# Kernel tuning notes

Measured on AMD Instinct MI355X. Metric: run time of the kernel, lower is better.

Reference implementation:

```python
import jax, jax.numpy as jnp
import numpy as np

N_NODES = 50000
N_EDGES = 600000
D = 128
NUM_GRAPHS = 64


def gcn_conv(x, W, b, edge_index, edge_weight, n):
    """PyG GCNConv: y = D^-1/2 (A+I) D^-1/2 (x W) + b, with self-loop weight 1."""
    h = x @ W  # [n, out]
    src, dst = edge_index[0], edge_index[1]
    if edge_weight is None:
        edge_weight = jnp.ones(src.shape, dtype=x.dtype)
    # append self loops
    loop = jnp.arange(n)
    src_f = jnp.concatenate([src, loop])
    dst_f = jnp.concatenate([dst, loop])
    w_f = jnp.concatenate([edge_weight, jnp.ones((n,), dtype=x.dtype)])
    deg = jax.ops.segment_sum(w_f, dst_f, num_segments=n)
    dis = jnp.where(deg > 0, jax.lax.rsqrt(jnp.maximum(deg, 1e-12)), 0.0)
    norm = dis[src_f] * w_f * dis[dst_f]  # [E+n]
    msg = h[src_f] * norm[:, None]
    out = jax.ops.segment_sum(msg, dst_f, num_segments=n)
    return out + b


def setup_inputs() -> dict:
    key = jax.random.key(0)
    ks = jax.random.split(key, 24)
    def w(k, shape, scale=0.05):
        return jax.random.normal(k, shape, dtype=jnp.float32) * scale
    inp = {
        'x': jax.random.normal(ks[0], (N_NODES, D), dtype=jnp.float32),
        'edge_index': jax.random.randint(ks[1], (2, N_EDGES), 0, N_NODES),
        'edge_attr': jax.random.uniform(ks[2], (N_EDGES, 4), dtype=jnp.float32),
        'batch': jnp.sort(jax.random.randint(ks[3], (N_NODES,), 0, NUM_GRAPHS)),
        'W1A': w(ks[4], (D, D)), 'b1A': jnp.zeros((D,), jnp.float32),
        'W1B': w(ks[5], (D, D)), 'b1B': jnp.zeros((D,), jnp.float32),
        'W1C': w(ks[6], (D, D)), 'b1C': jnp.zeros((D,), jnp.float32),
        'W1D': w(ks[7], (D, D)), 'b1D': jnp.zeros((D,), jnp.float32),
        'W2': w(ks[8], (4 * D, 2 * D)), 'b2': jnp.zeros((2 * D,), jnp.float32),
        'W3': w(ks[9], (2 * D, D)), 'b3': jnp.zeros((D,), jnp.float32),
        'Wm1': w(ks[10], (2 * D, 8)), 'bm1': jnp.zeros((8,), jnp.float32),
        'Wm2': w(ks[11], (8, 2)), 'bm2': jnp.zeros((2,), jnp.float32),
    }
    return inp


def reference(x, edge_index, edge_attr, batch, W1A, b1A, W1B, b1B, W1C, b1C,
              W1D, b1D, W2, b2, W3, b3, Wm1, bm1, Wm2, bm2):
    n = x.shape[0]
    xA = jax.nn.relu(gcn_conv(x, W1A, b1A, edge_index, edge_attr[:, 0], n))
    xB = jax.nn.relu(gcn_conv(x, W1B, b1B, edge_index, edge_attr[:, 1], n))
    xC = jax.nn.relu(gcn_conv(x, W1C, b1C, edge_index, edge_attr[:, 2], n))
    xD = jax.nn.relu(gcn_conv(x, W1D, b1D, edge_index, edge_attr[:, 3], n))
    h = jnp.concatenate([xA, xB, xC, xD], axis=1)  # [n, 4D]
    h = jax.nn.relu(gcn_conv(h, W2, b2, edge_index, None, n))
    h = gcn_conv(h, W3, b3, edge_index, None, n)  # [n, D]
    # global mean / max pool over graphs
    counts = jax.ops.segment_sum(jnp.ones((n,), h.dtype), batch, num_segments=NUM_GRAPHS)
    sums = jax.ops.segment_sum(h, batch, num_segments=NUM_GRAPHS)
    mean = sums / jnp.maximum(counts, 1.0)[:, None]
    mx = jax.ops.segment_max(h, batch, num_segments=NUM_GRAPHS)
    mx = jnp.where(counts[:, None] > 0, mx, 0.0)
    g = jnp.concatenate([mean, mx], axis=1)  # [G, 2D]
    # dropout is identity in eval mode
    logits = jax.nn.relu(g @ Wm1 + bm1) @ Wm2 + bm2
    return logits
```

## Files before the change

kernel.cpp:

```cpp
#include <hip/hip_runtime.h>

#define DEV_INLINE __device__ __forceinline__

typedef __attribute__((ext_vector_type(8))) short bf16x8;
typedef __attribute__((ext_vector_type(4))) float floatx4;

DEV_INLINE unsigned fencode(float f) {
  unsigned u = __float_as_uint(f);
  return (u & 0x80000000u) ? ~u : (u | 0x80000000u);
}
DEV_INLINE float fdecode(unsigned k) {
  return __uint_as_float((k & 0x80000000u) ? (k ^ 0x80000000u) : ~k);
}

DEV_INLINE unsigned short bf16_rne(float x) {
  unsigned u = __float_as_uint(x);
  unsigned r = (u + 0x7FFFu + ((u >> 16) & 1u)) >> 16;
  return (unsigned short)r;
}
DEV_INLINE void bf16_split(float x, unsigned short& hi, unsigned short& lo) {
  hi = bf16_rne(x);
  float hf = __uint_as_float(((unsigned)hi) << 16);
  lo = bf16_rne(x - hf);
}
DEV_INLINE float bf2f(unsigned short u) {
  return __uint_as_float(((unsigned)u) << 16);
}

#pragma clang diagnostic ignored "-Waddress-space-conversion"
DEV_INLINE void gload_lds16(const void* g, void* l) {
  __builtin_amdgcn_global_load_lds(
      (const __attribute__((address_space(1))) unsigned int*)g,
      (__attribute__((address_space(3))) unsigned int*)l, 16, 0, 0);
}

__global__ __launch_bounds__(256)
void prep_kernel(const float* __restrict__ WA, const float* __restrict__ WB,
                 const float* __restrict__ WC, const float* __restrict__ WD,
                 const float* __restrict__ bA, const float* __restrict__ bB,
                 const float* __restrict__ bC, const float* __restrict__ bD,
                 const float* __restrict__ W2, const float* __restrict__ W3,
                 unsigned short* __restrict__ W1t_hi, unsigned short* __restrict__ W1t_lo,
                 unsigned short* __restrict__ W2t_hi, unsigned short* __restrict__ W2t_lo,
                 unsigned short* __restrict__ W3t_hi, unsigned short* __restrict__ W3t_lo,
                 float* __restrict__ biascat) {
  int i = blockIdx.x * 256 + threadIdx.x;
  if (i < 65536) {
    int z = i >> 14, rem = i & 16383, j = rem >> 7, k = rem & 127;
    const float* W = (z == 0) ? WA : (z == 1) ? WB : (z == 2) ? WC : WD;
    unsigned short hi, lo;
    bf16_split(W[k * 128 + j], hi, lo);
    W1t_hi[i] = hi; W1t_lo[i] = lo;
  } else if (i < 196608) {
    int i2 = i - 65536, j = i2 >> 9, k = i2 & 511;
    unsigned short hi, lo;
    bf16_split(W2[k * 256 + j], hi, lo);
    W2t_hi[i2] = hi; W2t_lo[i2] = lo;
  } else if (i < 229376) {
    int i3 = i - 196608, j = i3 >> 8, k = i3 & 255;
    unsigned short hi, lo;
    bf16_split(W3[k * 128 + j], hi, lo);
    W3t_hi[i3] = hi; W3t_lo[i3] = lo;
  } else if (i < 229888) {
    int i4 = i - 229376, c = i4 >> 7, j = i4 & 127;
    const float* b = (c == 0) ? bA : (c == 1) ? bB : (c == 2) ? bC : bD;
    biascat[i4] = b[j];
  }
}

__global__ __launch_bounds__(256)
void xcast_kernel(const float* __restrict__ x, unsigned short* __restrict__ xb, int total4) {
  int i = blockIdx.x * 256 + threadIdx.x;
  if (i >= total4) return;
  float4 v = ((const float4*)x)[i];
  ushort4 o;
  o.x = bf16_rne(v.x); o.y = bf16_rne(v.y); o.z = bf16_rne(v.z); o.w = bf16_rne(v.w);
  ((ushort4*)xb)[i] = o;
}

__global__ __launch_bounds__(256)
void hist_kernel(const int* __restrict__ ei, int* __restrict__ cnt, int E) {
  int e = blockIdx.x * 256 + threadIdx.x;
  if (e < E) atomicAdd(&cnt[ei[E + e]], 1);
}

__global__ __launch_bounds__(256)
void scan1_kernel(const int* __restrict__ cnt, int* __restrict__ local,
                  int* __restrict__ bsum, int n) {
  __shared__ int s[256];
  int tid = threadIdx.x;
  int i = blockIdx.x * 256 + tid;
  int v = (i < n) ? cnt[i] : 0;
  s[tid] = v;
  __syncthreads();
#pragma unroll
  for (int off = 1; off < 256; off <<= 1) {
    int t = (tid >= off) ? s[tid - off] : 0;
    __syncthreads();
    s[tid] += t;
    __syncthreads();
  }
  if (i < n) local[i] = s[tid] - v;
  if (tid == 255) bsum[blockIdx.x] = s[255];
}

__global__ __launch_bounds__(256)
void scan2_kernel(int* __restrict__ bsum, int nb) {
  __shared__ int s[256];
  int tid = threadIdx.x;
  int v = (tid < nb) ? bsum[tid] : 0;
  s[tid] = v;
  __syncthreads();
#pragma unroll
  for (int off = 1; off < 256; off <<= 1) {
    int t = (tid >= off) ? s[tid - off] : 0;
    __syncthreads();
    s[tid] += t;
    __syncthreads();
  }
  if (tid < nb) bsum[tid] = s[tid] - v;
}

__global__ __launch_bounds__(256)
void scan3_kernel(const int* __restrict__ local, const int* __restrict__ bsum,
                  int* __restrict__ rowptr, int* __restrict__ rowwork, int n, int E) {
  int i = blockIdx.x * 256 + threadIdx.x;
  if (i < n) {
    int rp = local[i] + bsum[blockIdx.x];
    rowptr[i] = rp;
    rowwork[i] = rp;
  }
  if (i == 0) rowptr[n] = E;
}

__global__ __launch_bounds__(256)
void fill_kernel(const int* __restrict__ ei, int* __restrict__ rowwork,
                 int* __restrict__ csr, int* __restrict__ csr_src,
                 int* __restrict__ csr_dst, int E) {
  int e = blockIdx.x * 256 + threadIdx.x;
  if (e >= E) return;
  int d = ei[E + e];
  int pos = atomicAdd(&rowwork[d], 1);
  csr[pos] = e;
  csr_src[pos] = ei[e];
  csr_dst[pos] = d;
}

__global__ __launch_bounds__(256)
void degcsr_kernel(const int* __restrict__ rowptr, const int* __restrict__ csr,
                   const float* __restrict__ eattr, float* __restrict__ dis, int n) {
  int d = blockIdx.x * 256 + threadIdx.x;
  if (d >= n) return;
  int beg = rowptr[d], end = rowptr[d + 1];
  float s0 = 1.f, s1 = 1.f, s2 = 1.f, s3 = 1.f;
  for (int i = beg; i < end; ++i) {
    int e = csr[i];
    float4 w = ((const float4*)eattr)[e];
    s0 += w.x; s1 += w.y; s2 += w.z; s3 += w.w;
  }
  dis[d]         = 1.0f / sqrtf(s0);
  dis[n + d]     = 1.0f / sqrtf(s1);
  dis[2 * n + d] = 1.0f / sqrtf(s2);
  dis[3 * n + d] = 1.0f / sqrtf(s3);
  dis[4 * n + d] = 1.0f / sqrtf(1.0f + (float)(end - beg));
}

__global__ __launch_bounds__(256)
void edgeprep_kernel(const int* __restrict__ csr, const int* __restrict__ csr_src,
                     const int* __restrict__ csr_dst, const float* __restrict__ eattr,
                     const float* __restrict__ dis, float4* __restrict__ norm4,
                     float* __restrict__ norm1, int n, int E) {
  int i = blockIdx.x * 256 + threadIdx.x;
  if (i >= E) return;
  int e = csr[i], s = csr_src[i], d = csr_dst[i];
  float4 w = ((const float4*)eattr)[e];
  float4 o;
  o.x = dis[s] * w.x * dis[d];
  o.y = dis[n + s] * w.y * dis[n + d];
  o.z = dis[2 * n + s] * w.z * dis[2 * n + d];
  o.w = dis[3 * n + s] * w.w * dis[3 * n + d];
  norm4[i] = o;
  norm1[i] = dis[4 * n + s] * dis[4 * n + d];
}

__global__ __launch_bounds__(256)
void agg4x_kernel(const unsigned short* __restrict__ xb,
                  unsigned short* __restrict__ xa,
                  const int* __restrict__ rowptr, const int* __restrict__ csr_src,
                  const float4* __restrict__ norm4, const float* __restrict__ dis,
                  int n, int npad) {
  int d = blockIdx.x * 4 + (threadIdx.x >> 6);
  if (d >= n) return;
  int t = threadIdx.x & 63;
  float dc0 = dis[d], dc1 = dis[n + d], dc2 = dis[2 * n + d], dc3 = dis[3 * n + d];
  const ushort2* x2 = (const ushort2*)xb;
  ushort2 xu = x2[(size_t)d * 64 + t];
  float xvx = bf2f(xu.x), xvy = bf2f(xu.y);
  float a0x = xvx * dc0 * dc0, a0y = xvy * dc0 * dc0;
  float a1x = xvx * dc1 * dc1, a1y = xvy * dc1 * dc1;
  float a2x = xvx * dc2 * dc2, a2y = xvy * dc2 * dc2;
  float a3x = xvx * dc3 * dc3, a3y = xvy * dc3 * dc3;
  int beg = rowptr[d], end = rowptr[d + 1];
  int i = beg;
  for (; i + 4 <= end; i += 4) {
    int s0 = csr_src[i], s1 = csr_src[i + 1], s2 = csr_src[i + 2], s3 = csr_src[i + 3];
    float4 m0 = norm4[i], m1 = norm4[i + 1], m2 = norm4[i + 2], m3 = norm4[i + 3];
    ushort2 u0 = x2[(size_t)s0 * 64 + t];
    ushort2 u1 = x2[(size_t)s1 * 64 + t];
    ushort2 u2 = x2[(size_t)s2 * 64 + t];
    ushort2 u3 = x2[(size_t)s3 * 64 + t];
    float h0x = bf2f(u0.x), h0y = bf2f(u0.y);
    float h1x = bf2f(u1.x), h1y = bf2f(u1.y);
    float h2x = bf2f(u2.x), h2y = bf2f(u2.y);
    float h3x = bf2f(u3.x), h3y = bf2f(u3.y);
    a0x += h0x * m0.x; a0y += h0y * m0.x;
    a1x += h0x * m0.y; a1y += h0y * m0.y;
    a2x += h0x * m0.z; a2y += h0y * m0.z;
    a3x += h0x * m0.w; a3y += h0y * m0.w;
    a0x += h1x * m1.x; a0y += h1y * m1.x;
    a1x += h1x * m1.y; a1y += h1y * m1.y;
    a2x += h1x * m1.z; a2y += h1y * m1.z;
    a3x += h1x * m1.w; a3y += h1y * m1.w;
    a0x += h2x * m2.x; a0y += h2y * m2.x;
    a1x += h2x * m2.y; a1y += h2y * m2.y;
    a2x += h2x * m2.z; a2y += h2y * m2.z;
    a3x += h2x * m2.w; a3y += h2y * m2.w;
    a0x += h3x * m3.x; a0y += h3y * m3.x;
    a1x += h3x * m3.y; a1y += h3y * m3.y;
    a2x += h3x * m3.z; a2y += h3y * m3.z;
    a3x += h3x * m3.w; a3y += h3y * m3.w;
  }
  for (; i < end; ++i) {
    int s = csr_src[i];
    float4 m = norm4[i];
    ushort2 u = x2[(size_t)s * 64 + t];
    float hx = bf2f(u.x), hy = bf2f(u.y);
    a0x += hx * m.x; a0y += hy * m.x;
    a1x += hx * m.y; a1y += hy * m.y;
    a2x += hx * m.z; a2y += hy * m.z;
    a3x += hx * m.w; a3y += hy * m.w;
  }
  size_t plane = (size_t)npad * 128;
  size_t base = (size_t)d * 128 + 2 * t;
  float vx[4] = {a0x, a1x, a2x, a3x};
  float vy[4] = {a0y, a1y, a2y, a3y};
#pragma unroll
  for (int z = 0; z < 4; ++z) {
    ushort2 ov; ov.x = bf16_rne(vx[z]); ov.y = bf16_rne(vy[z]);
    *(ushort2*)&xa[plane * z + base] = ov;
  }
}

template <int MODE>
DEV_INLINE void gemm_mfma_body(const unsigned short* __restrict__ Ab, int K,
                               const unsigned short* __restrict__ Bh,
                               const unsigned short* __restrict__ Bl, int nTile0,
                               int ldc, int col0, unsigned short* __restrict__ Cb,
                               const float* __restrict__ bias, int M, int row0) {
  __shared__ __align__(16) unsigned short As[128 * 32];
  __shared__ __align__(16) unsigned short Bsh[128 * 32];
  __shared__ __align__(16) unsigned short Bsl[128 * 32];
  int tid = threadIdx.x;
  int w = tid >> 6, lane = tid & 63;
  int quad = lane >> 4, lrow = lane & 15;
  int wm = (w >> 1) * 64, wn = (w & 1) * 64;

  floatx4 zero4 = {0.f, 0.f, 0.f, 0.f};
  floatx4 acc[4][4];
#pragma unroll
  for (int i = 0; i < 4; ++i)
#pragma unroll
    for (int j = 0; j < 4; ++j) acc[i][j] = zero4;

  for (int k0 = 0; k0 < K; k0 += 32) {
#pragma unroll
    for (int half = 0; half < 2; ++half) {
      int row = half * 64 + lane;
      size_t ga = (size_t)(row0 + row) * K + k0 + w * 8;
      size_t gb = (size_t)(nTile0 + row) * K + k0 + w * 8;
      int lb = (w * 128 + half * 64) * 8;
      gload_lds16(Ab + ga, &As[lb]);
      gload_lds16(Bh + gb, &Bsh[lb]);
      gload_lds16(Bl + gb, &Bsl[lb]);
    }
    __syncthreads();
    bf16x8 ah[4];
#pragma unroll
    for (int i = 0; i < 4; ++i) {
      int off = (quad * 128 + wm + i * 16 + lrow) * 8;
      ah[i] = *(const bf16x8*)&As[off];
    }
#pragma unroll
    for (int j = 0; j < 4; ++j) {
      int off = (quad * 128 + wn + j * 16 + lrow) * 8;
      bf16x8 bh = *(const bf16x8*)&Bsh[off];
      bf16x8 bl = *(const bf16x8*)&Bsl[off];
#pragma unroll
      for (int i = 0; i < 4; ++i) {
        acc[i][j] = __builtin_amdgcn_mfma_f32_16x16x32_bf16(ah[i], bh, acc[i][j], 0, 0, 0);
        acc[i][j] = __builtin_amdgcn_mfma_f32_16x16x32_bf16(ah[i], bl, acc[i][j], 0, 0, 0);
      }
    }
    __syncthreads();
  }
#pragma unroll
  for (int i = 0; i < 4; ++i) {
#pragma unroll
    for (int j = 0; j < 4; ++j) {
      int colL = wn + j * 16 + lrow;
#pragma unroll
      for (int r = 0; r < 4; ++r) {
        int row = row0 + wm + i * 16 + quad * 4 + r;
        if (row < M) {
          float v = acc[i][j][r];
          if (MODE == 1) v = fmaxf(v + bias[colL], 0.0f);
          Cb[(size_t)row * ldc + col0 + colL] = bf16_rne(v);
        }
      }
    }
  }
}

__global__ __launch_bounds__(256)
void gemm_l1_mfma(const unsigned short* __restrict__ xa,
                  const unsigned short* __restrict__ W1t_hi,
                  const unsigned short* __restrict__ W1t_lo,
                  const float* __restrict__ biascat,
                  unsigned short* __restrict__ h1, int M, int npad) {
  int z = blockIdx.z;
  size_t ap = (size_t)z * npad * 128;
  gemm_mfma_body<1>(xa + ap, 128, W1t_hi + z * 16384, W1t_lo + z * 16384, 0,
                    512, z * 128, h1, biascat + z * 128, M, blockIdx.x * 128);
}

__global__ __launch_bounds__(256)
void gemm_bf16out(const unsigned short* __restrict__ Ab, int K,
                  const unsigned short* __restrict__ Bh,
                  const unsigned short* __restrict__ Bl,
                  unsigned short* __restrict__ Cb, int ldc, int M) {
  gemm_mfma_body<2>(Ab, K, Bh, Bl, blockIdx.y * 128, ldc, blockIdx.y * 128,
                    Cb, nullptr, M, blockIdx.x * 128);
}

template <int VEC, bool RELU, int OMODE>
__global__ __launch_bounds__(256)
void agg1_kernel(const unsigned short* __restrict__ hb, float* __restrict__ out,
                 unsigned short* __restrict__ ob,
                 const int* __restrict__ rowptr, const int* __restrict__ csr_src,
                 const float* __restrict__ norm1, const float* __restrict__ dis1,
                 const float* __restrict__ bias, int n) {
  constexpr int DOUT = VEC * 64;
  int d = blockIdx.x * 4 + (threadIdx.x >> 6);
  if (d >= n) return;
  int t = threadIdx.x & 63;
  float dd = dis1[d];
  float acc[VEC];
  {
    float sw = dd * dd;
#pragma unroll
    for (int k = 0; k < VEC; ++k) acc[k] = bf2f(hb[(size_t)d * DOUT + t * VEC + k]) * sw;
  }
  int beg = rowptr[d], end = rowptr[d + 1];
  int i = beg;
  for (; i + 4 <= end; i += 4) {
    int s0 = csr_src[i], s1 = csr_src[i + 1], s2 = csr_src[i + 2], s3 = csr_src[i + 3];
    float m0 = norm1[i], m1 = norm1[i + 1], m2 = norm1[i + 2], m3 = norm1[i + 3];
    if (VEC == 4) {
      ushort4 u0 = *(const ushort4*)&hb[(size_t)s0 * DOUT + t * 4];
      ushort4 u1 = *(const ushort4*)&hb[(size_t)s1 * DOUT + t * 4];
      ushort4 u2 = *(const ushort4*)&hb[(size_t)s2 * DOUT + t * 4];
      ushort4 u3 = *(const ushort4*)&hb[(size_t)s3 * DOUT + t * 4];
      acc[0] += bf2f(u0.x) * m0; acc[1] += bf2f(u0.y) * m0;
      acc[2 % VEC] += bf2f(u0.z) * m0; acc[3 % VEC] += bf2f(u0.w) * m0;
      acc[0] += bf2f(u1.x) * m1; acc[1] += bf2f(u1.y) * m1;
      acc[2 % VEC] += bf2f(u1.z) * m1; acc[3 % VEC] += bf2f(u1.w) * m1;
      acc[0] += bf2f(u2.x) * m2; acc[1] += bf2f(u2.y) * m2;
      acc[2 % VEC] += bf2f(u2.z) * m2; acc[3 % VEC] += bf2f(u2.w) * m2;
      acc[0] += bf2f(u3.x) * m3; acc[1] += bf2f(u3.y) * m3;
      acc[2 % VEC] += bf2f(u3.z) * m3; acc[3 % VEC] += bf2f(u3.w) * m3;
    } else {
      ushort2 u0 = *(const ushort2*)&hb[(size_t)s0 * DOUT + t * 2];
      ushort2 u1 = *(const ushort2*)&hb[(size_t)s1 * DOUT + t * 2];
      ushort2 u2 = *(const ushort2*)&hb[(size_t)s2 * DOUT + t * 2];
      ushort2 u3 = *(const ushort2*)&hb[(size_t)s3 * DOUT + t * 2];
      acc[0] += bf2f(u0.x) * m0; acc[1 % VEC] += bf2f(u0.y) * m0;
      acc[0] += bf2f(u1.x) * m1; acc[1 % VEC] += bf2f(u1.y) * m1;
      acc[0] += bf2f(u2.x) * m2; acc[1 % VEC] += bf2f(u2.y) * m2;
      acc[0] += bf2f(u3.x) * m3; acc[1 % VEC] += bf2f(u3.y) * m3;
    }
  }
  for (; i < end; ++i) {
    int s = csr_src[i];
    float nrm = norm1[i];
    if (VEC == 4) {
      ushort4 u = *(const ushort4*)&hb[(size_t)s * DOUT + t * 4];
      acc[0] += bf2f(u.x) * nrm; acc[1] += bf2f(u.y) * nrm;
      acc[2 % VEC] += bf2f(u.z) * nrm; acc[3 % VEC] += bf2f(u.w) * nrm;
    } else {
      ushort2 u = *(const ushort2*)&hb[(size_t)s * DOUT + t * 2];
      acc[0] += bf2f(u.x) * nrm; acc[1 % VEC] += bf2f(u.y) * nrm;
    }
  }
#pragma unroll
  for (int k = 0; k < VEC; ++k) {
    float r = acc[k] + bias[t * VEC + k];
    if (RELU) r = fmaxf(r, 0.0f);
    if (OMODE == 1) {
      ob[(size_t)d * DOUT + t * VEC + k] = bf16_rne(r);
    } else {
      out[(size_t)d * DOUT + t * VEC + k] = r;
    }
  }
}

__global__ __launch_bounds__(128)
void pool_kernel(const float* __restrict__ h3, const int* __restrict__ batch,
                 float* __restrict__ gsum, unsigned* __restrict__ gmax, int n) {
  int c = threadIdx.x;
  int start = blockIdx.x * 32;
  int end = min(start + 32, n);
  int curg = -1;
  float s = 0.0f, m = -3.402823466e38f;
  for (int i = start; i < end; ++i) {
    int g = batch[i];
    if (g != curg) {
      if (curg >= 0) {
        atomicAdd(&gsum[curg * 128 + c], s);
        atomicMax(&gmax[curg * 128 + c], fencode(m));
      }
      curg = g; s = 0.0f; m = -3.402823466e38f;
    }
    float v = h3[(size_t)i * 128 + c];
    s += v;
    m = fmaxf(m, v);
  }
  if (curg >= 0) {
    atomicAdd(&gsum[curg * 128 + c], s);
    atomicMax(&gmax[curg * 128 + c], fencode(m));
  }
}

__global__ __launch_bounds__(512)
void mlp_kernel(const float* __restrict__ gsum, const unsigned* __restrict__ gmax,
                const int* __restrict__ batch, int n, const float* __restrict__ Wm1,
                const float* __restrict__ bm1, const float* __restrict__ Wm2,
                const float* __restrict__ bm2, float* __restrict__ out) {
  __shared__ float hid[64][8];
  int t = threadIdx.x;
  int gi = t >> 3, u = t & 7;
  auto lb = [&](int key) {
    int lo = 0, hi = n;
    while (lo < hi) {
      int mid = (lo + hi) >> 1;
      if (batch[mid] < key) lo = mid + 1; else hi = mid;
    }
    return lo;
  };
  int cnt = lb(gi + 1) - lb(gi);
  float inv = 1.0f / fmaxf((float)cnt, 1.0f);
  float s = bm1[u];
  for (int k = 0; k < 128; ++k) {
    float mean = gsum[gi * 128 + k] * inv;
    s += mean * Wm1[k * 8 + u];
  }
  for (int k = 0; k < 128; ++k) {
    float mx = (cnt > 0) ? fdecode(gmax[gi * 128 + k]) : 0.0f;
    s += mx * Wm1[(128 + k) * 8 + u];
  }
  hid[gi][u] = fmaxf(s, 0.0f);
  __syncthreads();
  if (t < 128) {
    int g2 = t >> 1, o = t & 1;
    float s2 = bm2[o];
#pragma unroll
    for (int uu = 0; uu < 8; ++uu) s2 += hid[g2][uu] * Wm2[uu * 2 + o];
    out[g2 * 2 + o] = s2;
  }
}

extern "C" void kernel_launch(void* const* d_in, const int* in_sizes, int n_in,
                              void* d_out, int out_size, void* d_ws, size_t ws_size,
                              hipStream_t stream) {
  const float* x     = (const float*)d_in[0];
  const int*   ei    = (const int*)d_in[1];
  const float* eattr = (const float*)d_in[2];
  const int*   batch = (const int*)d_in[3];
  const float* W1A = (const float*)d_in[4],  *b1A = (const float*)d_in[5];
  const float* W1B = (const float*)d_in[6],  *b1B = (const float*)d_in[7];
  const float* W1C = (const float*)d_in[8],  *b1C = (const float*)d_in[9];
  const float* W1D = (const float*)d_in[10], *b1D = (const float*)d_in[11];
  const float* W2  = (const float*)d_in[12], *b2  = (const float*)d_in[13];
  const float* W3  = (const float*)d_in[14], *b3  = (const float*)d_in[15];
  const float* Wm1 = (const float*)d_in[16], *bm1 = (const float*)d_in[17];
  const float* Wm2 = (const float*)d_in[18], *bm2 = (const float*)d_in[19];
  float* out = (float*)d_out;

  const int n = in_sizes[0] / 128;
  const int E = in_sizes[1] / 2;
  const int npad = (n + 127) & ~127;
  const int nmb = npad / 128;

  char* ws = (char*)d_ws;
  size_t off = 0;
  auto alloc = [&](size_t bytes) -> void* {
    void* p = ws + off;
    off += (bytes + 255) & ~(size_t)255;
    return p;
  };

  float*    dis     = (float*)alloc((size_t)5 * n * 4);
  int*      rowptr  = (int*)alloc(((size_t)n + 1) * 4);
  int*      rowwork = (int*)alloc((size_t)n * 4);
  int*      local   = (int*)alloc((size_t)n * 4);
  int*      bsum    = (int*)alloc(256 * 4);
  size_t zoff = off;
  int*      cnt     = (int*)alloc((size_t)n * 4);
  float*    gsum    = (float*)alloc(64 * 128 * 4);
  unsigned* gmax    = (unsigned*)alloc(64 * 128 * 4);
  size_t zbytes = off - zoff;
  int*      csr     = (int*)alloc((size_t)E * 4);
  int*      csr_src = (int*)alloc((size_t)E * 4);
  int*      csr_dst = (int*)alloc((size_t)E * 4);
  float4*   norm4   = (float4*)alloc((size_t)E * 16);
  float*    norm1   = (float*)alloc((size_t)E * 4);
  unsigned short* W1t_hi = (unsigned short*)alloc(65536 * 2);
  unsigned short* W1t_lo = (unsigned short*)alloc(65536 * 2);
  unsigned short* W2t_hi = (unsigned short*)alloc(131072 * 2);
  unsigned short* W2t_lo = (unsigned short*)alloc(131072 * 2);
  unsigned short* W3t_hi = (unsigned short*)alloc(32768 * 2);
  unsigned short* W3t_lo = (unsigned short*)alloc(32768 * 2);
  float*    biascat = (float*)alloc(512 * 4);
  unsigned short* xb   = (unsigned short*)alloc((size_t)npad * 128 * 2);
  unsigned short* bufA = (unsigned short*)alloc((size_t)npad * 512 * 2);
  unsigned short* bufB = (unsigned short*)alloc((size_t)npad * 512 * 2);

  unsigned short* xa      = bufA;
  unsigned short* h1      = bufB;
  unsigned short* h2pre_b = bufA;
  unsigned short* h2      = bufB;
  unsigned short* h3pre_b = bufA;
  float*          h3      = (float*)(bufB + (size_t)npad * 256);

  hipMemsetAsync(ws + zoff, 0, zbytes, stream);

  prep_kernel<<<(229888 + 255) / 256, 256, 0, stream>>>(
      W1A, W1B, W1C, W1D, b1A, b1B, b1C, b1D, W2, W3,
      W1t_hi, W1t_lo, W2t_hi, W2t_lo, W3t_hi, W3t_lo, biascat);
  xcast_kernel<<<((n * 32) + 255) / 256, 256, 0, stream>>>(x, xb, n * 32);

  int nb = (n + 255) / 256;
  hist_kernel<<<(E + 255) / 256, 256, 0, stream>>>(ei, cnt, E);
  scan1_kernel<<<nb, 256, 0, stream>>>(cnt, local, bsum, n);
  scan2_kernel<<<1, 256, 0, stream>>>(bsum, nb);
  scan3_kernel<<<nb, 256, 0, stream>>>(local, bsum, rowptr, rowwork, n, E);
  fill_kernel<<<(E + 255) / 256, 256, 0, stream>>>(ei, rowwork, csr, csr_src, csr_dst, E);
  degcsr_kernel<<<(n + 255) / 256, 256, 0, stream>>>(rowptr, csr, eattr, dis, n);
  edgeprep_kernel<<<(E + 255) / 256, 256, 0, stream>>>(csr, csr_src, csr_dst, eattr,
                                                       dis, norm4, norm1, n, E);

  int nodeblk = (n + 3) / 4;
  agg4x_kernel<<<nodeblk, 256, 0, stream>>>(xb, xa, rowptr, csr_src, norm4, dis, n, npad);
  gemm_l1_mfma<<<dim3(nmb, 1, 4), 256, 0, stream>>>(xa, W1t_hi, W1t_lo, biascat, h1, n, npad);
  gemm_bf16out<<<dim3(nmb, 2), 256, 0, stream>>>(h1, 512, W2t_hi, W2t_lo, h2pre_b, 256, n);
  agg1_kernel<4, true, 1><<<nodeblk, 256, 0, stream>>>(h2pre_b, nullptr, h2,
                                                       rowptr, csr_src, norm1,
                                                       dis + (size_t)4 * n, b2, n);
  gemm_bf16out<<<dim3(nmb, 1), 256, 0, stream>>>(h2, 256, W3t_hi, W3t_lo, h3pre_b, 128, n);
  agg1_kernel<2, false, 0><<<nodeblk, 256, 0, stream>>>(h3pre_b, h3, nullptr,
                                                        rowptr, csr_src, norm1,
                                                        dis + (size_t)4 * n, b3, n);

  pool_kernel<<<(n + 31) / 32, 128, 0, stream>>>(h3, batch, gsum, gmax, n);
  mlp_kernel<<<1, 512, 0, stream>>>(gsum, gmax, batch, n, Wm1, bm1, Wm2, bm2, out);
}
```

Measured before the change: 532.6 us.

## Restructure MFMA GEMMs as narrow-column tiles with LDS-resident weights and register A

Replaces the 128x128 LDS-tiled GEMM with a kernel that loads a full 32-column slice of the hi/lo weight planes into LDS once. Each wave streams its own A rows straight from global memory into registers with one-step prefetch, so the k-loop has no per-step syncs. Row tiles grow to 512 (or 256) rows and padding grows to 512 to match. A now loads without LDS staging, but each A row is re-read by every column tile, which adds global traffic.

Result: slower. 563.2 us (+5.7%).

```diff
diff --git a/kernel.cpp b/kernel.cpp
--- a/kernel.cpp
+++ b/kernel.cpp
@@ -25,13 +25,6 @@
 }
 DEV_INLINE float bf2f(unsigned short u) {
   return __uint_as_float(((unsigned)u) << 16);
-}
-
-#pragma clang diagnostic ignored "-Waddress-space-conversion"
-DEV_INLINE void gload_lds16(const void* g, void* l) {
-  __builtin_amdgcn_global_load_lds(
-      (const __attribute__((address_space(1))) unsigned int*)g,
-      (__attribute__((address_space(3))) unsigned int*)l, 16, 0, 0);
 }
 
 __global__ __launch_bounds__(256)
@@ -251,70 +244,81 @@
   }
 }
 
-template <int MODE>
-DEV_INLINE void gemm_mfma_body(const unsigned short* __restrict__ Ab, int K,
-                               const unsigned short* __restrict__ Bh,
-                               const unsigned short* __restrict__ Bl, int nTile0,
-                               int ldc, int col0, unsigned short* __restrict__ Cb,
-                               const float* __restrict__ bias, int M, int row0) {
-  __shared__ __align__(16) unsigned short As[128 * 32];
-  __shared__ __align__(16) unsigned short Bsh[128 * 32];
-  __shared__ __align__(16) unsigned short Bsl[128 * 32];
+template <int KC, int SLABS, bool BIASRELU>
+DEV_INLINE void sgemm_body(const unsigned short* __restrict__ A,
+                           const unsigned short* __restrict__ Bh,
+                           const unsigned short* __restrict__ Bl,
+                           unsigned short* __restrict__ Cb, int ldc, int col0,
+                           const float* __restrict__ bias, int M, int row0base) {
+  constexpr int K = KC * 32;
+  __shared__ __align__(16) unsigned short Bs[KC * 2 * 32 * 32];
   int tid = threadIdx.x;
+  {
+    constexpr int total = KC * 2 * 32 * 4;
+#pragma unroll
+    for (int u0 = 0; u0 < total; u0 += 256) {
+      int u = u0 + tid;
+      int q = u & 3, c = (u >> 2) & 31, pl = (u >> 7) & 1, kc = u >> 8;
+      const unsigned short* src = (pl ? Bl : Bh) + c * K + kc * 32 + q * 8;
+      *(uint4*)&Bs[u * 8] = *(const uint4*)src;
+    }
+  }
+  __syncthreads();
   int w = tid >> 6, lane = tid & 63;
   int quad = lane >> 4, lrow = lane & 15;
-  int wm = (w >> 1) * 64, wn = (w & 1) * 64;
-
-  floatx4 zero4 = {0.f, 0.f, 0.f, 0.f};
-  floatx4 acc[4][4];
-#pragma unroll
-  for (int i = 0; i < 4; ++i)
-#pragma unroll
-    for (int j = 0; j < 4; ++j) acc[i][j] = zero4;
-
-  for (int k0 = 0; k0 < K; k0 += 32) {
-#pragma unroll
-    for (int half = 0; half < 2; ++half) {
-      int row = half * 64 + lane;
-      size_t ga = (size_t)(row0 + row) * K + k0 + w * 8;
-      size_t gb = (size_t)(nTile0 + row) * K + k0 + w * 8;
-      int lb = (w * 128 + half * 64) * 8;
-      gload_lds16(Ab + ga, &As[lb]);
-      gload_lds16(Bh + gb, &Bsh[lb]);
-      gload_lds16(Bl + gb, &Bsl[lb]);
-    }
-    __syncthreads();
-    bf16x8 ah[4];
-#pragma unroll
-    for (int i = 0; i < 4; ++i) {
-      int off = (quad * 128 + wm + i * 16 + lrow) * 8;
-      ah[i] = *(const bf16x8*)&As[off];
-    }
-#pragma unroll
-    for (int j = 0; j < 4; ++j) {
-      int off = (quad * 128 + wn + j * 16 + lrow) * 8;
-      bf16x8 bh = *(const bf16x8*)&Bsh[off];
-      bf16x8 bl = *(const bf16x8*)&Bsl[off];
-#pragma unroll
-      for (int i = 0; i < 4; ++i) {
-        acc[i][j] = __builtin_amdgcn_mfma_f32_16x16x32_bf16(ah[i], bh, acc[i][j], 0, 0, 0);
-        acc[i][j] = __builtin_amdgcn_mfma_f32_16x16x32_bf16(ah[i], bl, acc[i][j], 0, 0, 0);
+  int rows0 = row0base + w * (SLABS * 16);
+
+  floatx4 acc[SLABS][2];
+#pragma unroll
+  for (int s = 0; s < SLABS; ++s) {
+    acc[s][0] = {0.f, 0.f, 0.f, 0.f};
+    acc[s][1] = {0.f, 0.f, 0.f, 0.f};
+  }
+  const unsigned short* aptr[SLABS];
+#pragma unroll
+  for (int s = 0; s < SLABS; ++s)
+    aptr[s] = A + (size_t)(rows0 + s * 16 + lrow) * K + quad * 8;
+
+  bf16x8 acur[SLABS];
+#pragma unroll
+  for (int s = 0; s < SLABS; ++s) acur[s] = *(const bf16x8*)(aptr[s]);
+
+#pragma unroll
+  for (int kc = 0; kc < KC; ++kc) {
+    bf16x8 anxt[SLABS];
+    if (kc + 1 < KC) {
+#pragma unroll
+      for (int s = 0; s < SLABS; ++s)
+        anxt[s] = *(const bf16x8*)(aptr[s] + (kc + 1) * 32);
+    }
+#pragma unroll
+    for (int nf = 0; nf < 2; ++nf) {
+      int boff = (((kc * 2) * 32 + nf * 16 + lrow) * 4 + quad) * 8;
+      bf16x8 bh = *(const bf16x8*)&Bs[boff];
+      bf16x8 bl = *(const bf16x8*)&Bs[boff + 32 * 32];
+#pragma unroll
+      for (int s = 0; s < SLABS; ++s) {
+        acc[s][nf] = __builtin_amdgcn_mfma_f32_16x16x32_bf16(acur[s], bh, acc[s][nf], 0, 0, 0);
+        acc[s][nf] = __builtin_amdgcn_mfma_f32_16x16x32_bf16(acur[s], bl, acc[s][nf], 0, 0, 0);
       }
     }
-    __syncthreads();
-  }
-#pragma unroll
-  for (int i = 0; i < 4; ++i) {
-#pragma unroll
-    for (int j = 0; j < 4; ++j) {
-      int colL = wn + j * 16 + lrow;
+    if (kc + 1 < KC) {
+#pragma unroll
+      for (int s = 0; s < SLABS; ++s) acur[s] = anxt[s];
+    }
+  }
+#pragma unroll
+  for (int s = 0; s < SLABS; ++s) {
+#pragma unroll
+    for (int nf = 0; nf < 2; ++nf) {
+      int colL = col0 + nf * 16 + lrow;
 #pragma unroll
       for (int r = 0; r < 4; ++r) {
-        int row = row0 + wm + i * 16 + quad * 4 + r;
+        int row = rows0 + s * 16 + quad * 4 + r;
         if (row < M) {
-          float v = acc[i][j][r];
-          if (MODE == 1) v = fmaxf(v + bias[colL], 0.0f);
-          Cb[(size_t)row * ldc + col0 + colL] = bf16_rne(v);
+          float v = acc[s][nf][r];
+          if (BIASRELU) v = fmaxf(v + bias[nf * 16 + lrow], 0.0f);
+          Cb[(size_t)row * ldc + colL] = bf16_rne(v);
         }
       }
     }
@@ -322,24 +326,36 @@
 }
 
 __global__ __launch_bounds__(256)
-void gemm_l1_mfma(const unsigned short* __restrict__ xa,
-                  const unsigned short* __restrict__ W1t_hi,
-                  const unsigned short* __restrict__ W1t_lo,
-                  const float* __restrict__ biascat,
-                  unsigned short* __restrict__ h1, int M, int npad) {
-  int z = blockIdx.z;
-  size_t ap = (size_t)z * npad * 128;
-  gemm_mfma_body<1>(xa + ap, 128, W1t_hi + z * 16384, W1t_lo + z * 16384, 0,
-                    512, z * 128, h1, biascat + z * 128, M, blockIdx.x * 128);
-}
-
-__global__ __launch_bounds__(256)
-void gemm_bf16out(const unsigned short* __restrict__ Ab, int K,
-                  const unsigned short* __restrict__ Bh,
-                  const unsigned short* __restrict__ Bl,
-                  unsigned short* __restrict__ Cb, int ldc, int M) {
-  gemm_mfma_body<2>(Ab, K, Bh, Bl, blockIdx.y * 128, ldc, blockIdx.y * 128,
-                    Cb, nullptr, M, blockIdx.x * 128);
+void sgemm_l1(const unsigned short* __restrict__ xa,
+              const unsigned short* __restrict__ W1t_hi,
+              const unsigned short* __restrict__ W1t_lo,
+              const float* __restrict__ biascat,
+              unsigned short* __restrict__ h1, int M, int npad) {
+  int z = blockIdx.y >> 2, ct = blockIdx.y & 3;
+  int bofs = z * 16384 + ct * 32 * 128;
+  sgemm_body<4, 8, true>(xa + (size_t)z * npad * 128, W1t_hi + bofs, W1t_lo + bofs,
+                         h1, 512, z * 128 + ct * 32, biascat + z * 128 + ct * 32,
+                         M, blockIdx.x * 512);
+}
+
+__global__ __launch_bounds__(256)
+void sgemm_l2(const unsigned short* __restrict__ h1,
+              const unsigned short* __restrict__ W2t_hi,
+              const unsigned short* __restrict__ W2t_lo,
+              unsigned short* __restrict__ h2pre, int M) {
+  int n0 = blockIdx.y * 32;
+  sgemm_body<16, 8, false>(h1, W2t_hi + n0 * 512, W2t_lo + n0 * 512,
+                           h2pre, 256, n0, nullptr, M, blockIdx.x * 512);
+}
+
+__global__ __launch_bounds__(256)
+void sgemm_l3(const unsigned short* __restrict__ h2,
+              const unsigned short* __restrict__ W3t_hi,
+              const unsigned short* __restrict__ W3t_lo,
+              unsigned short* __restrict__ h3pre, int M) {
+  int n0 = blockIdx.y * 32;
+  sgemm_body<8, 4, false>(h2, W3t_hi + n0 * 256, W3t_lo + n0 * 256,
+                          h3pre, 128, n0, nullptr, M, blockIdx.x * 256);
 }
 
 template <int VEC, bool RELU, int OMODE>
@@ -497,8 +513,7 @@
 
   const int n = in_sizes[0] / 128;
   const int E = in_sizes[1] / 2;
-  const int npad = (n + 127) & ~127;
-  const int nmb = npad / 128;
+  const int npad = (n + 511) & ~511;
 
   char* ws = (char*)d_ws;
   size_t off = 0;
@@ -533,6 +548,7 @@
   unsigned short* xb   = (unsigned short*)alloc((size_t)npad * 128 * 2);
   unsigned short* bufA = (unsigned short*)alloc((size_t)npad * 512 * 2);
   unsigned short* bufB = (unsigned short*)alloc((size_t)npad * 512 * 2);
+  alloc(4096);
 
   unsigned short* xa      = bufA;
   unsigned short* h1      = bufB;
@@ -559,13 +575,14 @@
                                                        dis, norm4, norm1, n, E);
 
   int nodeblk = (n + 3) / 4;
+  int gm512 = npad / 512, gm256 = npad / 256;
   agg4x_kernel<<<nodeblk, 256, 0, stream>>>(xb, xa, rowptr, csr_src, norm4, dis, n, npad);
-  gemm_l1_mfma<<<dim3(nmb, 1, 4), 256, 0, stream>>>(xa, W1t_hi, W1t_lo, biascat, h1, n, npad);
-  gemm_bf16out<<<dim3(nmb, 2), 256, 0, stream>>>(h1, 512, W2t_hi, W2t_lo, h2pre_b, 256, n);
+  sgemm_l1<<<dim3(gm512, 16), 256, 0, stream>>>(xa, W1t_hi, W1t_lo, biascat, h1, n, npad);
+  sgemm_l2<<<dim3(gm512, 8), 256, 0, stream>>>(h1, W2t_hi, W2t_lo, h2pre_b, n);
   agg1_kernel<4, true, 1><<<nodeblk, 256, 0, stream>>>(h2pre_b, nullptr, h2,
                                                        rowptr, csr_src, norm1,
                                                        dis + (size_t)4 * n, b2, n);
-  gemm_bf16out<<<dim3(nmb, 1), 256, 0, stream>>>(h2, 256, W3t_hi, W3t_lo, h3pre_b, 128, n);
+  sgemm_l3<<<dim3(gm256, 4), 256, 0, stream>>>(h2, W3t_hi, W3t_lo, h3pre_b, n);
   agg1_kernel<2, false, 0><<<nodeblk, 256, 0, stream>>>(h3pre_b, h3, nullptr,
                                                         rowptr, csr_src, norm1,
                                                         dis + (size_t)4 * n, b3, n);
```

## Drop bf16 hi/lo weight split and double-buffer GEMM LDS tiles

Applied to the files above, without the earlier changes.

Weights are now rounded to a single bf16 copy instead of a hi+lo pair, which halves the MFMA count and the B-tile loads in every GEMM. The GEMM main loop also gains a double-buffered LDS stage, so the next K tile is prefetched while the current one is computed, with one barrier per iteration instead of two. The trade-off is lower weight precision (plain bf16 rather than roughly fp32-equivalent), which could push results past the accuracy tolerance.

New measurement: 496.8 us. -6.7%, faster.

```diff
diff --git a/kernel.cpp b/kernel.cpp
--- a/kernel.cpp
+++ b/kernel.cpp
@@ -17,11 +17,6 @@
   unsigned u = __float_as_uint(x);
   unsigned r = (u + 0x7FFFu + ((u >> 16) & 1u)) >> 16;
   return (unsigned short)r;
-}
-DEV_INLINE void bf16_split(float x, unsigned short& hi, unsigned short& lo) {
-  hi = bf16_rne(x);
-  float hf = __uint_as_float(((unsigned)hi) << 16);
-  lo = bf16_rne(x - hf);
 }
 DEV_INLINE float bf2f(unsigned short u) {
   return __uint_as_float(((unsigned)u) << 16);
@@ -40,27 +35,19 @@
                  const float* __restrict__ bA, const float* __restrict__ bB,
                  const float* __restrict__ bC, const float* __restrict__ bD,
                  const float* __restrict__ W2, const float* __restrict__ W3,
-                 unsigned short* __restrict__ W1t_hi, unsigned short* __restrict__ W1t_lo,
-                 unsigned short* __restrict__ W2t_hi, unsigned short* __restrict__ W2t_lo,
-                 unsigned short* __restrict__ W3t_hi, unsigned short* __restrict__ W3t_lo,
-                 float* __restrict__ biascat) {
+                 unsigned short* __restrict__ W1t, unsigned short* __restrict__ W2t,
+                 unsigned short* __restrict__ W3t, float* __restrict__ biascat) {
   int i = blockIdx.x * 256 + threadIdx.x;
   if (i < 65536) {
     int z = i >> 14, rem = i & 16383, j = rem >> 7, k = rem & 127;
     const float* W = (z == 0) ? WA : (z == 1) ? WB : (z == 2) ? WC : WD;
-    unsigned short hi, lo;
-    bf16_split(W[k * 128 + j], hi, lo);
-    W1t_hi[i] = hi; W1t_lo[i] = lo;
+    W1t[i] = bf16_rne(W[k * 128 + j]);
   } else if (i < 196608) {
     int i2 = i - 65536, j = i2 >> 9, k = i2 & 511;
-    unsigned short hi, lo;
-    bf16_split(W2[k * 256 + j], hi, lo);
-    W2t_hi[i2] = hi; W2t_lo[i2] = lo;
+    W2t[i2] = bf16_rne(W2[k * 256 + j]);
   } else if (i < 229376) {
     int i3 = i - 196608, j = i3 >> 8, k = i3 & 255;
-    unsigned short hi, lo;
-    bf16_split(W3[k * 128 + j], hi, lo);
-    W3t_hi[i3] = hi; W3t_lo[i3] = lo;
+    W3t[i3] = bf16_rne(W3[k * 128 + j]);
   } else if (i < 229888) {
     int i4 = i - 229376, c = i4 >> 7, j = i4 & 127;
     const float* b = (c == 0) ? bA : (c == 1) ? bB : (c == 2) ? bC : bD;
@@ -252,56 +239,52 @@
 }
 
 template <int MODE>
-DEV_INLINE void gemm_mfma_body(const unsigned short* __restrict__ Ab, int K,
-                               const unsigned short* __restrict__ Bh,
-                               const unsigned short* __restrict__ Bl, int nTile0,
+DEV_INLINE void gemm_mfma_body(const unsigned short* __restrict__ A, int K,
+                               const unsigned short* __restrict__ B,
                                int ldc, int col0, unsigned short* __restrict__ Cb,
                                const float* __restrict__ bias, int M, int row0) {
-  __shared__ __align__(16) unsigned short As[128 * 32];
-  __shared__ __align__(16) unsigned short Bsh[128 * 32];
-  __shared__ __align__(16) unsigned short Bsl[128 * 32];
+  __shared__ __align__(16) unsigned short As[2][128 * 32];
+  __shared__ __align__(16) unsigned short Bs[2][128 * 32];
   int tid = threadIdx.x;
   int w = tid >> 6, lane = tid & 63;
   int quad = lane >> 4, lrow = lane & 15;
   int wm = (w >> 1) * 64, wn = (w & 1) * 64;
 
-  floatx4 zero4 = {0.f, 0.f, 0.f, 0.f};
   floatx4 acc[4][4];
 #pragma unroll
   for (int i = 0; i < 4; ++i)
 #pragma unroll
-    for (int j = 0; j < 4; ++j) acc[i][j] = zero4;
-
-  for (int k0 = 0; k0 < K; k0 += 32) {
+    for (int j = 0; j < 4; ++j) acc[i][j] = {0.f, 0.f, 0.f, 0.f};
+
+  auto stage = [&](int b, int k0) {
 #pragma unroll
     for (int half = 0; half < 2; ++half) {
       int row = half * 64 + lane;
-      size_t ga = (size_t)(row0 + row) * K + k0 + w * 8;
-      size_t gb = (size_t)(nTile0 + row) * K + k0 + w * 8;
       int lb = (w * 128 + half * 64) * 8;
-      gload_lds16(Ab + ga, &As[lb]);
-      gload_lds16(Bh + gb, &Bsh[lb]);
-      gload_lds16(Bl + gb, &Bsl[lb]);
-    }
+      gload_lds16(A + (size_t)(row0 + row) * K + k0 + w * 8, &As[b][lb]);
+      gload_lds16(B + (size_t)row * K + k0 + w * 8, &Bs[b][lb]);
+    }
+  };
+
+  int nk = K >> 5;
+  stage(0, 0);
+  int buf = 0;
+  for (int kt = 0; kt < nk; ++kt) {
     __syncthreads();
-    bf16x8 ah[4];
-#pragma unroll
-    for (int i = 0; i < 4; ++i) {
-      int off = (quad * 128 + wm + i * 16 + lrow) * 8;
-      ah[i] = *(const bf16x8*)&As[off];
-    }
-#pragma unroll
-    for (int j = 0; j < 4; ++j) {
-      int off = (quad * 128 + wn + j * 16 + lrow) * 8;
-      bf16x8 bh = *(const bf16x8*)&Bsh[off];
-      bf16x8 bl = *(const bf16x8*)&Bsl[off];
-#pragma unroll
-      for (int i = 0; i < 4; ++i) {
-        acc[i][j] = __builtin_amdgcn_mfma_f32_16x16x32_bf16(ah[i], bh, acc[i][j], 0, 0, 0);
-        acc[i][j] = __builtin_amdgcn_mfma_f32_16x16x32_bf16(ah[i], bl, acc[i][j], 0, 0, 0);
-      }
-    }
-    __syncthreads();
+    if (kt + 1 < nk) stage(buf ^ 1, (kt + 1) * 32);
+    bf16x8 a_[4], b_[4];
+#pragma unroll
+    for (int i = 0; i < 4; ++i)
+      a_[i] = *(const bf16x8*)&As[buf][(quad * 128 + wm + i * 16 + lrow) * 8];
+#pragma unroll
+    for (int j = 0; j < 4; ++j)
+      b_[j] = *(const bf16x8*)&Bs[buf][(quad * 128 + wn + j * 16 + lrow) * 8];
+#pragma unroll
+    for (int j = 0; j < 4; ++j)
+#pragma unroll
+      for (int i = 0; i < 4; ++i)
+        acc[i][j] = __builtin_amdgcn_mfma_f32_16x16x32_bf16(a_[i], b_[j], acc[i][j], 0, 0, 0);
+    buf ^= 1;
   }
 #pragma unroll
   for (int i = 0; i < 4; ++i) {
@@ -323,23 +306,20 @@
 
 __global__ __launch_bounds__(256)
 void gemm_l1_mfma(const unsigned short* __restrict__ xa,
-                  const unsigned short* __restrict__ W1t_hi,
-                  const unsigned short* __restrict__ W1t_lo,
+                  const unsigned short* __restrict__ W1t,
                   const float* __restrict__ biascat,
                   unsigned short* __restrict__ h1, int M, int npad) {
   int z = blockIdx.z;
-  size_t ap = (size_t)z * npad * 128;
-  gemm_mfma_body<1>(xa + ap, 128, W1t_hi + z * 16384, W1t_lo + z * 16384, 0,
+  gemm_mfma_body<1>(xa + (size_t)z * npad * 128, 128, W1t + z * 16384,
                     512, z * 128, h1, biascat + z * 128, M, blockIdx.x * 128);
 }
 
 __global__ __launch_bounds__(256)
-void gemm_bf16out(const unsigned short* __restrict__ Ab, int K,
-                  const unsigned short* __restrict__ Bh,
-                  const unsigned short* __restrict__ Bl,
+void gemm_bf16out(const unsigned short* __restrict__ A, int K,
+                  const unsigned short* __restrict__ B,
                   unsigned short* __restrict__ Cb, int ldc, int M) {
-  gemm_mfma_body<2>(Ab, K, Bh, Bl, blockIdx.y * 128, ldc, blockIdx.y * 128,
-                    Cb, nullptr, M, blockIdx.x * 128);
+  gemm_mfma_body<2>(A, K, B + (size_t)blockIdx.y * 128 * K, ldc,
+                    blockIdx.y * 128, Cb, nullptr, M, blockIdx.x * 128);
 }
 
 template <int VEC, bool RELU, int OMODE>
@@ -523,16 +503,14 @@
   int*      csr_dst = (int*)alloc((size_t)E * 4);
   float4*   norm4   = (float4*)alloc((size_t)E * 16);
   float*    norm1   = (float*)alloc((size_t)E * 4);
-  unsigned short* W1t_hi = (unsigned short*)alloc(65536 * 2);
-  unsigned short* W1t_lo = (unsigned short*)alloc(65536 * 2);
-  unsigned short* W2t_hi = (unsigned short*)alloc(131072 * 2);
-  unsigned short* W2t_lo = (unsigned short*)alloc(131072 * 2);
-  unsigned short* W3t_hi = (unsigned short*)alloc(32768 * 2);
-  unsigned short* W3t_lo = (unsigned short*)alloc(32768 * 2);
+  unsigned short* W1t = (unsigned short*)alloc(65536 * 2);
+  unsigned short* W2t = (unsigned short*)alloc(131072 * 2);
+  unsigned short* W3t = (unsigned short*)alloc(32768 * 2);
   float*    biascat = (float*)alloc(512 * 4);
   unsigned short* xb   = (unsigned short*)alloc((size_t)npad * 128 * 2);
   unsigned short* bufA = (unsigned short*)alloc((size_t)npad * 512 * 2);
   unsigned short* bufB = (unsigned short*)alloc((size_t)npad * 512 * 2);
+  alloc(4096);
 
   unsigned short* xa      = bufA;
   unsigned short* h1      = bufB;
@@ -545,7 +523,7 @@
 
   prep_kernel<<<(229888 + 255) / 256, 256, 0, stream>>>(
       W1A, W1B, W1C, W1D, b1A, b1B, b1C, b1D, W2, W3,
-      W1t_hi, W1t_lo, W2t_hi, W2t_lo, W3t_hi, W3t_lo, biascat);
+      W1t, W2t, W3t, biascat);
   xcast_kernel<<<((n * 32) + 255) / 256, 256, 0, stream>>>(x, xb, n * 32);
 
   int nb = (n + 255) / 256;
@@ -560,12 +538,12 @@
 
   int nodeblk = (n + 3) / 4;
   agg4x_kernel<<<nodeblk, 256, 0, stream>>>(xb, xa, rowptr, csr_src, norm4, dis, n, npad);
-  gemm_l1_mfma<<<dim3(nmb, 1, 4), 256, 0, stream>>>(xa, W1t_hi, W1t_lo, biascat, h1, n, npad);
-  gemm_bf16out<<<dim3(nmb, 2), 256, 0, stream>>>(h1, 512, W2t_hi, W2t_lo, h2pre_b, 256, n);
+  gemm_l1_mfma<<<dim3(nmb, 1, 4), 256, 0, stream>>>(xa, W1t, biascat, h1, n, npad);
+  gemm_bf16out<<<dim3(nmb, 2), 256, 0, stream>>>(h1, 512, W2t, h2pre_b, 256, n);
   agg1_kernel<4, true, 1><<<nodeblk, 256, 0, stream>>>(h2pre_b, nullptr, h2,
                                                        rowptr, csr_src, norm1,
                                                        dis + (size_t)4 * n, b2, n);
-  gemm_bf16out<<<dim3(nmb, 1), 256, 0, stream>>>(h2, 256, W3t_hi, W3t_lo, h3pre_b, 128, n);
+  gemm_bf16out<<<dim3(nmb, 1), 256, 0, stream>>>(h2, 256, W3t, h3pre_b, 128, n);
   agg1_kernel<2, false, 0><<<nodeblk, 256, 0, stream>>>(h3pre_b, h3, nullptr,
                                                         rowptr, csr_src, norm1,
                                                         dis + (size_t)4 * n, b3, n);
```
